# Performance work log

Measured on AMD Instinct MI355X. Metric: run time of the kernel, lower is better.

## Reference

```python
import jax, jax.numpy as jnp
import numpy as np

N_OBJ, C_DET, C_SEG, H, W = 1024, 8, 4, 28, 28


def setup_inputs() -> dict:
    key = jax.random.key(0)
    k1, k2, k3 = jax.random.split(key, 3)
    # probabilities exactly as produced upstream in forward():
    # det class probs = logits.softmax(1); det masks = sigmoid probs;
    # seg masks = softmax over seg_class axis (axis=2)
    det_class_probs = jax.nn.softmax(jax.random.normal(k1, (N_OBJ, C_DET)), axis=1)
    det_mask_probs = jax.nn.sigmoid(jax.random.normal(k2, (N_OBJ, C_DET, H, W)))
    seg_mask_probs = jax.nn.softmax(jax.random.normal(k3, (N_OBJ, C_DET, C_SEG, H, W)), axis=2)
    # bipartite graph edges (seg_class i, det_class j), distinct pairs
    edges = np.array([(i, j) for j in range(C_DET) for i in range(C_SEG) if (i + j) % 2 == 0],
                     dtype=np.int64)
    edge_i = jnp.asarray(edges[:, 0])
    edge_j = jnp.asarray(edges[:, 1])
    return {
        'det_class_probs': det_class_probs,
        'det_mask_probs': det_mask_probs,
        'seg_mask_probs': seg_mask_probs,
        'edge_i': edge_i,
        'edge_j': edge_j,
    }


def reference(det_class_probs, det_mask_probs, seg_mask_probs, edge_i, edge_j):
    # Per edge (i, j):
    #   area   = sum_{n,h,w} seg[:, j, i] * det[:, j]
    #   p_area = area / sum_{n,h,w} det[:, j]
    #   p_i_j  = p_area * det_class_probs[:, j]          (shape (N_obj,))
    # probs = sum over edges of p_i_j.
    # Batch all edges: overlap matrix A[j, i] and denominator per det class.
    A = jnp.einsum('ncshw,nchw->cs', seg_mask_probs, det_mask_probs)  # (C_det, C_seg)
    denom = det_mask_probs.sum(axis=(0, 2, 3))                        # (C_det,)
    p_area = A / denom[:, None]                                       # (C_det, C_seg)
    # accumulate per-edge scalar weights onto their det class j
    w = jnp.zeros((A.shape[0],), A.dtype).at[edge_j].add(p_area[edge_j, edge_i])
    probs = det_class_probs @ w                                       # (N_obj,)
    # F.binary_cross_entropy(probs, ones) = mean(-log(probs)), log clamped at -100
    bce_loss = (-jnp.clip(jnp.log(probs), -100.0, None)).mean()
    return bce_loss
```

## Files before the change

kernel.cpp:

```cpp
#include <hip/hip_runtime.h>
#include <math.h>

#define N_OBJ 1024
#define C_DET 8
#define C_SEG 4
#define HW    784
#define HW4   196
#define NWS   (C_DET + C_DET * C_SEG)


__global__ void zero_ws_kernel(float* __restrict__ ws) {
    if (threadIdx.x < NWS) ws[threadIdx.x] = 0.f;
}

__global__ __launch_bounds__(256) void overlap_kernel(
    const float* __restrict__ det,
    const float* __restrict__ seg,
    float* __restrict__ ws)
{
    const int c = blockIdx.y;
    float accA0 = 0.f, accA1 = 0.f, accA2 = 0.f, accA3 = 0.f, accD = 0.f;

    const int total4 = N_OBJ * HW4;
    for (int t4 = blockIdx.x * blockDim.x + threadIdx.x; t4 < total4;
         t4 += gridDim.x * blockDim.x) {
        const int n  = t4 / HW4;
        const int p4 = t4 - n * HW4;
        const size_t drow = (size_t)(n * C_DET + c) * HW + (size_t)p4 * 4;
        const float4 d = *reinterpret_cast<const float4*>(det + drow);
        accD += (d.x + d.y) + (d.z + d.w);

        const size_t srow = (size_t)(n * C_DET + c) * (C_SEG * HW) + (size_t)p4 * 4;
        const float4 s0 = *reinterpret_cast<const float4*>(seg + srow + 0 * HW);
        const float4 s1 = *reinterpret_cast<const float4*>(seg + srow + 1 * HW);
        const float4 s2 = *reinterpret_cast<const float4*>(seg + srow + 2 * HW);
        const float4 s3 = *reinterpret_cast<const float4*>(seg + srow + 3 * HW);
        accA0 += s0.x * d.x + s0.y * d.y + s0.z * d.z + s0.w * d.w;
        accA1 += s1.x * d.x + s1.y * d.y + s1.z * d.z + s1.w * d.w;
        accA2 += s2.x * d.x + s2.y * d.y + s2.z * d.z + s2.w * d.w;
        accA3 += s3.x * d.x + s3.y * d.y + s3.z * d.z + s3.w * d.w;
    }

    __shared__ float sred[5][4];
    const int lane = threadIdx.x & 63;
    const int wv   = threadIdx.x >> 6;
    float vals[5] = {accD, accA0, accA1, accA2, accA3};
    #pragma unroll
    for (int k = 0; k < 5; ++k) {
        float v = vals[k];
        #pragma unroll
        for (int off = 32; off > 0; off >>= 1) v += __shfl_down(v, off, 64);
        if (lane == 0) sred[k][wv] = v;
    }
    __syncthreads();
    if (threadIdx.x < 5) {
        const float v = sred[threadIdx.x][0] + sred[threadIdx.x][1]
                      + sred[threadIdx.x][2] + sred[threadIdx.x][3];
        if (threadIdx.x == 0) atomicAdd(&ws[c], v);
        else atomicAdd(&ws[C_DET + c * C_SEG + (threadIdx.x - 1)], v);
    }
}

__global__ __launch_bounds__(256) void finalize_kernel(
    const float* __restrict__ det_class,
    const int* __restrict__ edge_i,
    const int* __restrict__ edge_j,
    const int n_edges,
    const float* __restrict__ ws,
    float* __restrict__ out)
{
    __shared__ float wsh[C_DET];
    if (threadIdx.x < C_DET) wsh[threadIdx.x] = 0.f;
    __syncthreads();
    if (threadIdx.x < n_edges) {
        const int i = edge_i[threadIdx.x];
        const int j = edge_j[threadIdx.x];
        atomicAdd(&wsh[j], ws[C_DET + j * C_SEG + i] / ws[j]);
    }
    __syncthreads();

    float wl[C_DET];
    #pragma unroll
    for (int k = 0; k < C_DET; ++k) wl[k] = wsh[k];

    float acc = 0.f;
    for (int n = threadIdx.x; n < N_OBJ; n += blockDim.x) {
        float p = 0.f;
        #pragma unroll
        for (int k = 0; k < C_DET; ++k)
            p += det_class[n * C_DET + k] * wl[k];
        const float lg = fmaxf(logf(p), -100.f);
        acc += -lg;
    }

    __shared__ float sred[4];
    const int lane = threadIdx.x & 63;
    const int wv   = threadIdx.x >> 6;
    float v = acc;
    #pragma unroll
    for (int off = 32; off > 0; off >>= 1) v += __shfl_down(v, off, 64);
    if (lane == 0) sred[wv] = v;
    __syncthreads();
    if (threadIdx.x == 0) {
        const float total = sred[0] + sred[1] + sred[2] + sred[3];
        out[0] = total * (1.0f / N_OBJ);
    }
}

extern "C" void kernel_launch(void* const* d_in, const int* in_sizes, int n_in,
                              void* d_out, int out_size, void* d_ws, size_t ws_size,
                              hipStream_t stream) {
    const float* det_class = (const float*)d_in[0];
    const float* det       = (const float*)d_in[1];
    const float* seg       = (const float*)d_in[2];
    const int*   edge_i    = (const int*)d_in[3];
    const int*   edge_j    = (const int*)d_in[4];
    const int    n_edges   = in_sizes[3];
    float* out = (float*)d_out;
    float* ws  = (float*)d_ws;

    zero_ws_kernel<<<1, 64, 0, stream>>>(ws);
    overlap_kernel<<<dim3(128, C_DET), 256, 0, stream>>>(det, seg, ws);
    finalize_kernel<<<1, 256, 0, stream>>>(det_class, edge_i, edge_j, n_edges, ws, out);
}
```

Before: 185.4 us.

## Replace atomics with per-block partials, drop zero kernel, use nontemporal loads

Each overlap block now writes its five partial sums to a dedicated workspace slot, and the finalize kernel reduces them, so the separate zero kernel launch and the global atomics go away. The streaming loads of det and seg use nontemporal builtins, the grid-stride loop is unrolled by two to keep more loads in flight, and the finalize kernel reads det_class as vectors. In exchange the finalize kernel runs a serial 128-element reduction on 40 threads.

```diff
diff --git a/kernel.cpp b/kernel.cpp
--- a/kernel.cpp
+++ b/kernel.cpp
@@ -6,40 +6,51 @@
 #define C_SEG 4
 #define HW    784
 #define HW4   196
-#define NWS   (C_DET + C_DET * C_SEG)
+#define NBLK  128
 
+typedef float f32x4 __attribute__((ext_vector_type(4)));
 
-__global__ void zero_ws_kernel(float* __restrict__ ws) {
-    if (threadIdx.x < NWS) ws[threadIdx.x] = 0.f;
-}
 
 __global__ __launch_bounds__(256) void overlap_kernel(
     const float* __restrict__ det,
     const float* __restrict__ seg,
-    float* __restrict__ ws)
+    float* __restrict__ partial)
 {
-    const int c = blockIdx.y;
-    float accA0 = 0.f, accA1 = 0.f, accA2 = 0.f, accA3 = 0.f, accD = 0.f;
+    const int c  = blockIdx.y;
+    const int bx = blockIdx.x;
+    float accD = 0.f, accA0 = 0.f, accA1 = 0.f, accA2 = 0.f, accA3 = 0.f;
 
     const int total4 = N_OBJ * HW4;
-    for (int t4 = blockIdx.x * blockDim.x + threadIdx.x; t4 < total4;
-         t4 += gridDim.x * blockDim.x) {
+    const int step   = NBLK * 256;
+
+    auto body = [&](int t4) {
         const int n  = t4 / HW4;
         const int p4 = t4 - n * HW4;
-        const size_t drow = (size_t)(n * C_DET + c) * HW + (size_t)p4 * 4;
-        const float4 d = *reinterpret_cast<const float4*>(det + drow);
-        accD += (d.x + d.y) + (d.z + d.w);
-
-        const size_t srow = (size_t)(n * C_DET + c) * (C_SEG * HW) + (size_t)p4 * 4;
-        const float4 s0 = *reinterpret_cast<const float4*>(seg + srow + 0 * HW);
-        const float4 s1 = *reinterpret_cast<const float4*>(seg + srow + 1 * HW);
-        const float4 s2 = *reinterpret_cast<const float4*>(seg + srow + 2 * HW);
-        const float4 s3 = *reinterpret_cast<const float4*>(seg + srow + 3 * HW);
+        const int drow = (n * C_DET + c) * HW + p4 * 4;
+        const f32x4 d = __builtin_nontemporal_load(
+            reinterpret_cast<const f32x4*>(det + drow));
+        const int srow = (n * C_DET + c) * (C_SEG * HW) + p4 * 4;
+        const f32x4 s0 = __builtin_nontemporal_load(
+            reinterpret_cast<const f32x4*>(seg + srow + 0 * HW));
+        const f32x4 s1 = __builtin_nontemporal_load(
+            reinterpret_cast<const f32x4*>(seg + srow + 1 * HW));
+        const f32x4 s2 = __builtin_nontemporal_load(
+            reinterpret_cast<const f32x4*>(seg + srow + 2 * HW));
+        const f32x4 s3 = __builtin_nontemporal_load(
+            reinterpret_cast<const f32x4*>(seg + srow + 3 * HW));
+        accD  += (d.x + d.y) + (d.z + d.w);
         accA0 += s0.x * d.x + s0.y * d.y + s0.z * d.z + s0.w * d.w;
         accA1 += s1.x * d.x + s1.y * d.y + s1.z * d.z + s1.w * d.w;
         accA2 += s2.x * d.x + s2.y * d.y + s2.z * d.z + s2.w * d.w;
         accA3 += s3.x * d.x + s3.y * d.y + s3.z * d.z + s3.w * d.w;
+    };
+
+    int t4 = bx * 256 + threadIdx.x;
+    for (; t4 + step < total4; t4 += 2 * step) {
+        body(t4);
+        body(t4 + step);
     }
+    if (t4 < total4) body(t4);
 
     __shared__ float sred[5][4];
     const int lane = threadIdx.x & 63;
@@ -56,8 +67,7 @@
     if (threadIdx.x < 5) {
         const float v = sred[threadIdx.x][0] + sred[threadIdx.x][1]
                       + sred[threadIdx.x][2] + sred[threadIdx.x][3];
-        if (threadIdx.x == 0) atomicAdd(&ws[c], v);
-        else atomicAdd(&ws[C_DET + c * C_SEG + (threadIdx.x - 1)], v);
+        partial[(c * NBLK + bx) * 5 + threadIdx.x] = v;
     }
 }
 
@@ -66,16 +76,30 @@
     const int* __restrict__ edge_i,
     const int* __restrict__ edge_j,
     const int n_edges,
-    const float* __restrict__ ws,
+    const float* __restrict__ partial,
     float* __restrict__ out)
 {
+    __shared__ float A[C_DET][C_SEG];
+    __shared__ float D[C_DET];
     __shared__ float wsh[C_DET];
-    if (threadIdx.x < C_DET) wsh[threadIdx.x] = 0.f;
+    const int tid = threadIdx.x;
+
+    if (tid < 40) {
+        const int c = tid / 5;
+        const int k = tid - c * 5;
+        float s = 0.f;
+        for (int b = 0; b < NBLK; ++b)
+            s += partial[(c * NBLK + b) * 5 + k];
+        if (k == 0) D[c] = s;
+        else        A[c][k - 1] = s;
+    }
+    if (tid < C_DET) wsh[tid] = 0.f;
     __syncthreads();
-    if (threadIdx.x < n_edges) {
-        const int i = edge_i[threadIdx.x];
-        const int j = edge_j[threadIdx.x];
-        atomicAdd(&wsh[j], ws[C_DET + j * C_SEG + i] / ws[j]);
+
+    if (tid < n_edges) {
+        const int i = edge_i[tid];
+        const int j = edge_j[tid];
+        atomicAdd(&wsh[j], A[j][i] / D[j]);
     }
     __syncthreads();
 
@@ -84,26 +108,24 @@
     for (int k = 0; k < C_DET; ++k) wl[k] = wsh[k];
 
     float acc = 0.f;
-    for (int n = threadIdx.x; n < N_OBJ; n += blockDim.x) {
-        float p = 0.f;
-        #pragma unroll
-        for (int k = 0; k < C_DET; ++k)
-            p += det_class[n * C_DET + k] * wl[k];
-        const float lg = fmaxf(logf(p), -100.f);
-        acc += -lg;
+    for (int n = tid; n < N_OBJ; n += 256) {
+        const f32x4 a = *reinterpret_cast<const f32x4*>(det_class + n * C_DET);
+        const f32x4 b = *reinterpret_cast<const f32x4*>(det_class + n * C_DET + 4);
+        float p = a.x * wl[0] + a.y * wl[1] + a.z * wl[2] + a.w * wl[3]
+                + b.x * wl[4] + b.y * wl[5] + b.z * wl[6] + b.w * wl[7];
+        acc += -fmaxf(logf(p), -100.f);
     }
 
     __shared__ float sred[4];
-    const int lane = threadIdx.x & 63;
-    const int wv   = threadIdx.x >> 6;
+    const int lane = tid & 63;
+    const int wv   = tid >> 6;
     float v = acc;
     #pragma unroll
     for (int off = 32; off > 0; off >>= 1) v += __shfl_down(v, off, 64);
     if (lane == 0) sred[wv] = v;
     __syncthreads();
-    if (threadIdx.x == 0) {
-        const float total = sred[0] + sred[1] + sred[2] + sred[3];
-        out[0] = total * (1.0f / N_OBJ);
+    if (tid == 0) {
+        out[0] = (sred[0] + sred[1] + sred[2] + sred[3]) * (1.0f / N_OBJ);
     }
 }
 
@@ -117,9 +139,9 @@
     const int*   edge_j    = (const int*)d_in[4];
     const int    n_edges   = in_sizes[3];
     float* out = (float*)d_out;
-    float* ws  = (float*)d_ws;
+    float* partial = (float*)d_ws;
 
-    zero_ws_kernel<<<1, 64, 0, stream>>>(ws);
-    overlap_kernel<<<dim3(128, C_DET), 256, 0, stream>>>(det, seg, ws);
-    finalize_kernel<<<1, 256, 0, stream>>>(det_class, edge_i, edge_j, n_edges, ws, out);
+    overlap_kernel<<<dim3(NBLK, C_DET), 256, 0, stream>>>(det, seg, partial);
+    finalize_kernel<<<1, 256, 0, stream>>>(det_class, edge_i, edge_j, n_edges,
+                                           partial, out);
 }
```

After: 175.5 us. 5.4% less time.
